# Kernel optimization log

Hardware: AMD Instinct MI355X
Metric: run time of the kernel (lower is better)

Reference implementation:

```python
import jax, jax.numpy as jnp
import numpy as np

N = 100000
E = 1600000
IN_CH = 128
HID = 64      # hidden_channels, heads=1 -> out_ch per head = 64
OUT = 40      # final classes, heads=1, concat=False -> mean over 1 head
SLOPE = 0.2   # leaky relu slope


def setup_inputs() -> dict:
    key = jax.random.key(0)
    k = jax.random.split(key, 6)
    x = jax.random.normal(k[0], (N, IN_CH), dtype=jnp.float32)
    edge_index = jax.random.randint(k[1], (2, E), 0, N, dtype=jnp.int32)
    # xavier-ish scales
    W0 = jax.random.normal(k[2], (HID, IN_CH), dtype=jnp.float32) * (2.0 / (HID + IN_CH)) ** 0.5
    att0 = jax.random.normal(k[3], (1, 1, 2 * HID), dtype=jnp.float32) * 0.1
    W1 = jax.random.normal(k[4], (OUT, HID), dtype=jnp.float32) * (2.0 / (OUT + HID)) ** 0.5
    att1 = jax.random.normal(k[5], (1, 1, 2 * OUT), dtype=jnp.float32) * 0.1
    return {"x": x, "edge_index": edge_index, "W0": W0, "att0": att0, "W1": W1, "att1": att1}


def _gat_conv(h_in, src, dst, W, att, out_ch, concat):
    # h_in: (N, in_ch) -> h: (N, 1, out_ch)   (heads = 1)
    h = (h_in @ W.T).reshape(N, 1, out_ch)
    x_i = h[dst]                                   # (Etot, 1, out_ch) target feats
    x_j = h[src]                                   # (Etot, 1, out_ch) source feats
    logits = jnp.sum(jnp.concatenate([x_i, x_j], axis=-1) * att, axis=-1)  # (Etot, 1)
    logits = jax.nn.leaky_relu(logits, negative_slope=SLOPE)
    # segment softmax over destination node
    m = jax.ops.segment_max(logits, dst, num_segments=N)
    e = jnp.exp(logits - m[dst])
    s = jax.ops.segment_sum(e, dst, num_segments=N)
    alpha = e / s[dst]                             # (Etot, 1)
    out = jax.ops.segment_sum(x_j * alpha[..., None], dst, num_segments=N)  # (N, 1, out_ch)
    return out.reshape(N, out_ch) if concat else out.mean(axis=1)


def reference(x, edge_index, W0, att0, W1, att1):
    # add_self_loops (applied inside each GATConv with the same node count)
    loops = jnp.arange(N, dtype=edge_index.dtype)
    ei = jnp.concatenate([edge_index, jnp.stack([loops, loops])], axis=1)
    src, dst = ei[0], ei[1]  # PyG source_to_target: x_j = x[src], x_i = x[dst]
    h = _gat_conv(x, src, dst, W0, att0, HID, concat=True)
    h = jax.nn.relu(h)  # dropout inactive in eval mode
    h = _gat_conv(h, src, dst, W1, att1, OUT, concat=False)
    return jax.nn.log_softmax(h, axis=1)
```

## Files before the change

kernel.cpp:

```cpp
#include <hip/hip_runtime.h>
#include <math.h>

#define NNODES 100000
#define NEDGES 1600000
#define ETOT   (NEDGES + NNODES)

#define BSZ   128
#define KBUCK ((NNODES + BSZ - 1) / BSZ)
#define CAP   2816
#define NSUB  8
#define CAPS  768
#define CPAD  16

#define GEMMB 1563
#define EPT   4
#define BUCKB ((ETOT + 1024 - 1) / 1024)
#define GGRP  ((GEMMB + 7) / 8)
#define BGRP  ((BUCKB + 7) / 8)

__device__ __forceinline__ int xcc_id() {
    int x;
    asm volatile("s_getreg_b32 %0, hwreg(HW_REG_XCC_ID)" : "=s"(x));
    return x & (NSUB - 1);
}

__device__ __forceinline__ unsigned short f2bf(float f) {
    unsigned u = __float_as_uint(f);
    return (unsigned short)((u + 0x7FFFu + ((u >> 16) & 1u)) >> 16);
}

__global__ void zero_cnt(int* __restrict__ cnt) {
    int i = blockIdx.x * blockDim.x + threadIdx.x;
    if (i < KBUCK * NSUB * CPAD) cnt[i] = 0;
}

__device__ __forceinline__ void bucket_body(int bb, const int* __restrict__ ei,
                                            int* __restrict__ cnt,
                                            unsigned int* __restrict__ stage) {
    const int t = threadIdx.x;
    const int xg = xcc_id();
#pragma unroll
    for (int r = 0; r < EPT; ++r) {
        int e = bb * 1024 + r * 256 + t;
        if (e < ETOT) {
            int src, dst;
            if (e < NEDGES) { src = ei[e]; dst = ei[NEDGES + e]; }
            else            { src = dst = e - NEDGES; }
            int sb = (dst >> 7) * NSUB + xg;
            int pos = atomicAdd(&cnt[sb * CPAD], 1);
            if (pos < CAPS)
                stage[(size_t)sb * CAPS + pos] =
                    ((unsigned)(dst & 127) << 24) | (unsigned)src;
        }
    }
}

__device__ __forceinline__ void gemm0_body(int gb, const float* __restrict__ x,
                                           const float* __restrict__ W,
                                           const float* __restrict__ att,
                                           unsigned short* __restrict__ h0b,
                                           float* __restrict__ ai,
                                           float* __restrict__ aj) {
    __shared__ float Wt[128 * 68];
    const int tid = threadIdx.x;
    const int nb = gb * 64;

    const int lane = tid & 63;
    const int w    = tid >> 6;
    const int ocg  = lane & 15;
    const int ng   = lane >> 4;
    const int nodeLocal = w * 16 + ng * 4;

    const float* xp[4];
#pragma unroll
    for (int j = 0; j < 4; ++j) {
        int node = nb + nodeLocal + j;
        xp[j] = x + (size_t)(node < NNODES ? node : NNODES - 1) * 128;
    }

    float4 xa[4], xb[4], xc[4];
#pragma unroll
    for (int j = 0; j < 4; ++j) {
        xa[j] = *(const float4*)(xp[j] + 0);
        xb[j] = *(const float4*)(xp[j] + 4);
        xc[j] = *(const float4*)(xp[j] + 8);
    }

    for (int i = tid; i < 128 * 64; i += 256) {
        int oc = i >> 7, k = i & 127;
        Wt[k * 68 + oc] = W[i];
    }
    __syncthreads();

    float4 acc[4];
#pragma unroll
    for (int j = 0; j < 4; ++j) acc[j] = make_float4(0.f, 0.f, 0.f, 0.f);

#pragma unroll 4
    for (int k4 = 0; k4 < 32; ++k4) {
        const int kb = k4 * 4;
        int kpf = kb + 12; if (kpf > 124) kpf = 124;
        float4 xn0 = *(const float4*)(xp[0] + kpf);
        float4 xn1 = *(const float4*)(xp[1] + kpf);
        float4 xn2 = *(const float4*)(xp[2] + kpf);
        float4 xn3 = *(const float4*)(xp[3] + kpf);
        float4 wv0 = *(const float4*)&Wt[(kb + 0) * 68 + ocg * 4];
        float4 wv1 = *(const float4*)&Wt[(kb + 1) * 68 + ocg * 4];
        float4 wv2 = *(const float4*)&Wt[(kb + 2) * 68 + ocg * 4];
        float4 wv3 = *(const float4*)&Wt[(kb + 3) * 68 + ocg * 4];
#pragma unroll
        for (int j = 0; j < 4; ++j) {
            float4 xv = xa[j];
            acc[j].x += xv.x * wv0.x + xv.y * wv1.x + xv.z * wv2.x + xv.w * wv3.x;
            acc[j].y += xv.x * wv0.y + xv.y * wv1.y + xv.z * wv2.y + xv.w * wv3.y;
            acc[j].z += xv.x * wv0.z + xv.y * wv1.z + xv.z * wv2.z + xv.w * wv3.z;
            acc[j].w += xv.x * wv0.w + xv.y * wv1.w + xv.z * wv2.w + xv.w * wv3.w;
        }
        xa[0] = xb[0]; xa[1] = xb[1]; xa[2] = xb[2]; xa[3] = xb[3];
        xb[0] = xc[0]; xb[1] = xc[1]; xb[2] = xc[2]; xb[3] = xc[3];
        xc[0] = xn0;   xc[1] = xn1;   xc[2] = xn2;   xc[3] = xn3;
    }

    const int ocb = ocg * 4;
    float ati[4], atj[4];
#pragma unroll
    for (int i = 0; i < 4; ++i) {
        ati[i] = att[ocb + i];
        atj[i] = att[64 + ocb + i];
    }

#pragma unroll
    for (int j = 0; j < 4; ++j) {
        int nodeG = nb + nodeLocal + j;
        float pai = acc[j].x * ati[0] + acc[j].y * ati[1] + acc[j].z * ati[2] + acc[j].w * ati[3];
        float paj = acc[j].x * atj[0] + acc[j].y * atj[1] + acc[j].z * atj[2] + acc[j].w * atj[3];
#pragma unroll
        for (int off = 1; off < 16; off <<= 1) {
            pai += __shfl_xor(pai, off, 64);
            paj += __shfl_xor(paj, off, 64);
        }
        if (nodeG < NNODES) {
            unsigned p0 = ((unsigned)f2bf(acc[j].y) << 16) | f2bf(acc[j].x);
            unsigned p1 = ((unsigned)f2bf(acc[j].w) << 16) | f2bf(acc[j].z);
            *(uint2*)&h0b[(size_t)nodeG * 64 + ocb] = make_uint2(p0, p1);
            if (ocg == 0) { ai[nodeG] = pai; aj[nodeG] = paj; }
        }
    }
}

__global__ __launch_bounds__(256) void fusedA(
        const int* __restrict__ ei, int* __restrict__ cnt,
        unsigned int* __restrict__ stage,
        const float* __restrict__ x, const float* __restrict__ W0,
        const float* __restrict__ att0,
        unsigned short* __restrict__ h0b, float* __restrict__ ai0,
        float* __restrict__ aj0) {
    const int bid = blockIdx.x;
    const int grp = bid >> 3, sub = bid & 7;
    if ((grp & 1) && (grp >> 1) < GGRP) {
        int g = (grp >> 1) * 8 + sub;
        if (g < GEMMB) gemm0_body(g, x, W0, att0, h0b, ai0, aj0);
    } else {
        int bg = grp - min(GGRP, (grp + 1) >> 1);
        int bb = bg * 8 + sub;
        if (bb < BUCKB) bucket_body(bb, ei, cnt, stage);
    }
}

__global__ void bucket_scan(const int* __restrict__ cnt, int* __restrict__ bstart) {
    __shared__ int wsum[16];
    const int t = threadIdx.x;
    int x = 0;
    if (t < KBUCK) {
#pragma unroll
        for (int s = 0; s < NSUB; ++s) x += min(cnt[(t * NSUB + s) * CPAD], CAPS);
    }
    int lane = t & 63, w = t >> 6;
    int inc = x;
#pragma unroll
    for (int off = 1; off < 64; off <<= 1) {
        int u = __shfl_up(inc, off, 64);
        if (lane >= off) inc += u;
    }
    if (lane == 63) wsum[w] = inc;
    __syncthreads();
    if (t == 0) {
        int s = 0;
#pragma unroll
        for (int j = 0; j < 16; ++j) { int y = wsum[j]; wsum[j] = s; s += y; }
    }
    __syncthreads();
    int excl = inc - x + wsum[w];
    if (t < KBUCK) bstart[t] = excl;
    if (t == KBUCK) bstart[KBUCK] = excl;
}

__global__ __launch_bounds__(256) void bucket_scatter(
        const int* __restrict__ cnt, const int* __restrict__ bstart,
        const unsigned int* __restrict__ stage, int* __restrict__ rowstart,
        int* __restrict__ csr_src) {
    __shared__ unsigned int ent[CAP];
    __shared__ int hist[BSZ];
    __shared__ int scnt[NSUB];
    __shared__ int soff[NSUB + 1];
    __shared__ int wtot;
    const int b = blockIdx.x, t = threadIdx.x;
    const int n0 = b * BSZ;
    const int base = bstart[b];

    if (t < BSZ) hist[t] = 0;
    if (t < NSUB) scnt[t] = min(cnt[(b * NSUB + t) * CPAD], CAPS);
    __syncthreads();
    if (t == 0) {
        int s = 0;
#pragma unroll
        for (int x = 0; x < NSUB; ++x) { soff[x] = s; s += scnt[x]; }
        soff[NSUB] = s;
    }
    __syncthreads();

#pragma unroll
    for (int x = 0; x < NSUB; ++x) {
        const int cx = scnt[x];
        const int ox = soff[x];
        const unsigned int* sp = stage + (size_t)(b * NSUB + x) * CAPS;
        for (int i = t; i < cx; i += 256) {
            unsigned int v = sp[i];
            ent[ox + i] = v;
            atomicAdd(&hist[v >> 24], 1);
        }
    }
    __syncthreads();
    const int c = soff[NSUB];

    int lane = t & 63, w = t >> 6;
    int v = (t < BSZ) ? hist[t] : 0;
    int inc = v;
#pragma unroll
    for (int off = 1; off < 64; off <<= 1) {
        int u = __shfl_up(inc, off, 64);
        if (lane >= off) inc += u;
    }
    if (t == 63) wtot = inc;
    __syncthreads();
    int excl = inc - v + ((w == 1) ? wtot : 0);
    if (t < BSZ) {
        int node = n0 + t;
        if (node <= NNODES) rowstart[node] = base + excl;
    }
    __syncthreads();
    if (t < BSZ) hist[t] = excl;
    __syncthreads();
    for (int i = t; i < c; i += 256) {
        unsigned int e = ent[i];
        int pos = atomicAdd(&hist[e >> 24], 1);
        csr_src[base + pos] = (int)(e & 0xFFFFFFu);
    }
}

__global__ __launch_bounds__(256) void agg_gemm1(
        const int* __restrict__ rowstart, const int* __restrict__ csr_src,
        const float* __restrict__ aj,
        const float* __restrict__ ai, const unsigned short* __restrict__ h0b,
        const float* __restrict__ W1, const float* __restrict__ att1,
        unsigned short* __restrict__ h1b, float* __restrict__ ai1,
        float* __restrict__ aj1) {
    __shared__ float  W1L[64 * 68];
    __shared__ float  rowbuf[4][64];

    const int tid = threadIdx.x;
    for (int i = tid; i < 64 * 64; i += 256) {
        int oc = i >> 6, k = i & 63;
        W1L[oc * 68 + k] = (oc < 40) ? W1[oc * 64 + k] : 0.0f;
    }
    __syncthreads();

    const int lane = tid & 63;
    const int wid  = tid >> 6;
    const int n = blockIdx.x * 4 + wid;
    if (n >= NNODES) return;

    const int start = rowstart[n];
    const int end   = rowstart[n + 1];
    const float ain = ai[n];

    const int cg = lane & 7;
    const int sg = lane >> 3;
    const int cgo = cg << 3;
    float4 accA = make_float4(0.f, 0.f, 0.f, 0.f);
    float4 accB = make_float4(0.f, 0.f, 0.f, 0.f);
    float  esum = 0.0f;

    for (int c = start; c < end; c += 64) {
        int rem = end - c;
        int cnt = (rem < 64) ? rem : 64;
        int s = (lane < cnt) ? csr_src[c + lane] : 0;
        for (int j0 = 0; j0 < cnt; j0 += 8) {
            int j  = j0 + sg;
            int sj = __shfl(s, j, 64);
            if (j < cnt) {
                float ajv = aj[sj];
                uint4 hv = *(const uint4*)&h0b[(unsigned)(sj << 6) + cgo];
                float t = ain + ajv;
                t = (t > 0.0f) ? t : 0.2f * t;
                float a = __expf(t);
                esum += a;
                float c0 = __uint_as_float(hv.x << 16);
                float c1 = __uint_as_float(hv.x & 0xFFFF0000u);
                float c2 = __uint_as_float(hv.y << 16);
                float c3 = __uint_as_float(hv.y & 0xFFFF0000u);
                float c4 = __uint_as_float(hv.z << 16);
                float c5 = __uint_as_float(hv.z & 0xFFFF0000u);
                float c6 = __uint_as_float(hv.w << 16);
                float c7 = __uint_as_float(hv.w & 0xFFFF0000u);
                accA.x = fmaf(a, c0, accA.x);
                accA.y = fmaf(a, c1, accA.y);
                accA.z = fmaf(a, c2, accA.z);
                accA.w = fmaf(a, c3, accA.w);
                accB.x = fmaf(a, c4, accB.x);
                accB.y = fmaf(a, c5, accB.y);
                accB.z = fmaf(a, c6, accB.z);
                accB.w = fmaf(a, c7, accB.w);
            }
        }
    }
#pragma unroll
    for (int off = 32; off > 0; off >>= 1) esum += __shfl_xor(esum, off, 64);
    const float inv = 8.0f / esum;
#pragma unroll
    for (int off = 8; off < 64; off <<= 1) {
        accA.x += __shfl_xor(accA.x, off, 64);
        accA.y += __shfl_xor(accA.y, off, 64);
        accA.z += __shfl_xor(accA.z, off, 64);
        accA.w += __shfl_xor(accA.w, off, 64);
        accB.x += __shfl_xor(accB.x, off, 64);
        accB.y += __shfl_xor(accB.y, off, 64);
        accB.z += __shfl_xor(accB.z, off, 64);
        accB.w += __shfl_xor(accB.w, off, 64);
    }
    if (sg == 0) {
        float4 rA, rB;
        rA.x = fmaxf(accA.x * inv, 0.0f);
        rA.y = fmaxf(accA.y * inv, 0.0f);
        rA.z = fmaxf(accA.z * inv, 0.0f);
        rA.w = fmaxf(accA.w * inv, 0.0f);
        rB.x = fmaxf(accB.x * inv, 0.0f);
        rB.y = fmaxf(accB.y * inv, 0.0f);
        rB.z = fmaxf(accB.z * inv, 0.0f);
        rB.w = fmaxf(accB.w * inv, 0.0f);
        *(float4*)&rowbuf[wid][cgo]     = rA;
        *(float4*)&rowbuf[wid][cgo + 4] = rB;
    }

    const int oc = lane;
    float hacc = 0.0f;
#pragma unroll
    for (int k4 = 0; k4 < 16; ++k4) {
        float4 rv = *(const float4*)&rowbuf[wid][k4 * 4];
        float4 wv = *(const float4*)&W1L[oc * 68 + k4 * 4];
        hacc = fmaf(rv.x, wv.x, hacc);
        hacc = fmaf(rv.y, wv.y, hacc);
        hacc = fmaf(rv.z, wv.z, hacc);
        hacc = fmaf(rv.w, wv.w, hacc);
    }

    const bool ocOK = (oc < 40);
    if (ocOK) h1b[(size_t)n * 40 + oc] = f2bf(hacc);
    float pai = ocOK ? hacc * att1[oc]      : 0.0f;
    float paj = ocOK ? hacc * att1[40 + oc] : 0.0f;
#pragma unroll
    for (int off = 1; off < 64; off <<= 1) {
        pai += __shfl_xor(pai, off, 64);
        paj += __shfl_xor(paj, off, 64);
    }
    if (lane == 0) { ai1[n] = pai; aj1[n] = paj; }
}

__global__ __launch_bounds__(256) void agg_lsm(
        const int* __restrict__ rowstart, const int* __restrict__ csr_src,
        const float* __restrict__ aj,
        const float* __restrict__ ai, const unsigned short* __restrict__ h1b,
        float* __restrict__ out) {
    const int lane = threadIdx.x & 63;
    const int wid  = threadIdx.x >> 6;
    const int n = blockIdx.x * 4 + wid;
    if (n >= NNODES) return;

    const int start = rowstart[n];
    const int end   = rowstart[n + 1];
    const float ain = ai[n];

    const int  cg   = lane & 7;
    const int  sg   = lane >> 3;
    const bool chOK = (cg < 5);
    float4 accA = make_float4(0.f, 0.f, 0.f, 0.f);
    float4 accB = make_float4(0.f, 0.f, 0.f, 0.f);
    float  esum = 0.0f;

    for (int c = start; c < end; c += 64) {
        int rem = end - c;
        int cnt = (rem < 64) ? rem : 64;
        int s = (lane < cnt) ? csr_src[c + lane] : 0;
        for (int j0 = 0; j0 < cnt; j0 += 8) {
            int j  = j0 + sg;
            int sj = __shfl(s, j, 64);
            if (j < cnt) {
                float ajv = aj[sj];
                float t = ain + ajv;
                t = (t > 0.0f) ? t : 0.2f * t;
                float a = __expf(t);
                esum += a;
                if (chOK) {
                    uint4 hv = *(const uint4*)&h1b[(unsigned)(sj * 40) + (cg << 3)];
                    float c0 = __uint_as_float(hv.x << 16);
                    float c1 = __uint_as_float(hv.x & 0xFFFF0000u);
                    float c2 = __uint_as_float(hv.y << 16);
                    float c3 = __uint_as_float(hv.y & 0xFFFF0000u);
                    float c4 = __uint_as_float(hv.z << 16);
                    float c5 = __uint_as_float(hv.z & 0xFFFF0000u);
                    float c6 = __uint_as_float(hv.w << 16);
                    float c7 = __uint_as_float(hv.w & 0xFFFF0000u);
                    accA.x = fmaf(a, c0, accA.x);
                    accA.y = fmaf(a, c1, accA.y);
                    accA.z = fmaf(a, c2, accA.z);
                    accA.w = fmaf(a, c3, accA.w);
                    accB.x = fmaf(a, c4, accB.x);
                    accB.y = fmaf(a, c5, accB.y);
                    accB.z = fmaf(a, c6, accB.z);
                    accB.w = fmaf(a, c7, accB.w);
                }
            }
        }
    }
#pragma unroll
    for (int off = 32; off > 0; off >>= 1) esum += __shfl_xor(esum, off, 64);
    const float inv = 8.0f / esum;
#pragma unroll
    for (int off = 8; off < 64; off <<= 1) {
        accA.x += __shfl_xor(accA.x, off, 64);
        accA.y += __shfl_xor(accA.y, off, 64);
        accA.z += __shfl_xor(accA.z, off, 64);
        accA.w += __shfl_xor(accA.w, off, 64);
        accB.x += __shfl_xor(accB.x, off, 64);
        accB.y += __shfl_xor(accB.y, off, 64);
        accB.z += __shfl_xor(accB.z, off, 64);
        accB.w += __shfl_xor(accB.w, off, 64);
    }
    accA.x *= inv; accA.y *= inv; accA.z *= inv; accA.w *= inv;
    accB.x *= inv; accB.y *= inv; accB.z *= inv; accB.w *= inv;

    float mx = -INFINITY;
    if (chOK) {
        mx = fmaxf(fmaxf(fmaxf(accA.x, accA.y), fmaxf(accA.z, accA.w)),
                   fmaxf(fmaxf(accB.x, accB.y), fmaxf(accB.z, accB.w)));
    }
#pragma unroll
    for (int off = 1; off < 8; off <<= 1) mx = fmaxf(mx, __shfl_xor(mx, off, 64));
    float sm = 0.0f;
    if (chOK) {
        sm = __expf(accA.x - mx) + __expf(accA.y - mx) +
             __expf(accA.z - mx) + __expf(accA.w - mx) +
             __expf(accB.x - mx) + __expf(accB.y - mx) +
             __expf(accB.z - mx) + __expf(accB.w - mx);
    }
#pragma unroll
    for (int off = 1; off < 8; off <<= 1) sm += __shfl_xor(sm, off, 64);
    float ls = mx + logf(sm);
    if (sg == 0 && chOK) {
        float4 oA = make_float4(accA.x - ls, accA.y - ls, accA.z - ls, accA.w - ls);
        float4 oB = make_float4(accB.x - ls, accB.y - ls, accB.z - ls, accB.w - ls);
        *(float4*)&out[(size_t)n * 40 + (cg << 3)]     = oA;
        *(float4*)&out[(size_t)n * 40 + (cg << 3) + 4] = oB;
    }
}

extern "C" void kernel_launch(void* const* d_in, const int* in_sizes, int n_in,
                              void* d_out, int out_size, void* d_ws, size_t ws_size,
                              hipStream_t stream) {
    const float* x    = (const float*)d_in[0];
    const int*   ei   = (const int*)  d_in[1];
    const float* W0   = (const float*)d_in[2];
    const float* att0 = (const float*)d_in[3];
    const float* W1   = (const float*)d_in[4];
    const float* att1 = (const float*)d_in[5];
    float* out = (float*)d_out;

    int* wi = (int*)d_ws;
    int*  cnt      = wi;
    int*  bstart   = cnt + 100352;
    int*  rowstart = bstart + 1024;
    unsigned int* stage = (unsigned int*)(rowstart + 100352);
    int*  csr_src  = (int*)(stage + (size_t)KBUCK * NSUB * CAPS);
    unsigned short* h0b = (unsigned short*)(csr_src + 1700096);
    unsigned short* h1b = h0b + (size_t)NNODES * 64;
    float* fbase = (float*)(h1b + (size_t)NNODES * 40);
    float* ai0 = fbase;
    float* aj0 = ai0 + 100352;
    float* ai1 = aj0 + 100352;
    float* aj1 = ai1 + 100352;

    const int B = 256;
    const int aggGrid = (NNODES + 3) / 4;
    const int fusedGrid = (GGRP + BGRP) * 8;

    zero_cnt<<<(KBUCK * NSUB * CPAD + B - 1) / B, B, 0, stream>>>(cnt);
    fusedA<<<fusedGrid, B, 0, stream>>>(ei, cnt, stage, x, W0, att0, h0b, ai0, aj0);
    bucket_scan<<<1, 1024, 0, stream>>>(cnt, bstart);
    bucket_scatter<<<KBUCK, B, 0, stream>>>(cnt, bstart, stage, rowstart, csr_src);

    agg_gemm1<<<aggGrid, B, 0, stream>>>(rowstart, csr_src, aj0, ai0, h0b,
                                         W1, att1, h1b, ai1, aj1);

    agg_lsm<<<aggGrid, B, 0, stream>>>(rowstart, csr_src, aj1, ai1, h1b, out);
}
```

Before: 378.5 us.

## Precompute per-edge attention exponentials into CSR arrays before aggregation

Computes the unnormalized attention weight exp(leakyrelu(ai+aj)) per edge once: layer 0 inside bucket_scatter, layer 1 in a new alpha1_k kernel. The results are stored alongside csr_src. The aggregation kernels then read a coalesced alpha value and broadcast it by shuffle. This removes the redundant per-lane exp evaluation, which previously ran once per channel group (hence the old 8/esum factor), and the scattered aj gather inside the aggregation loop. The cost is an extra kernel launch and extra CSR-sized float traffic, and the stage buffer is reused as storage for the layer-1 alphas.

```diff
diff --git a/kernel.cpp b/kernel.cpp
--- a/kernel.cpp
+++ b/kernel.cpp
@@ -198,9 +198,11 @@
 __global__ __launch_bounds__(256) void bucket_scatter(
         const int* __restrict__ cnt, const int* __restrict__ bstart,
         const unsigned int* __restrict__ stage, int* __restrict__ rowstart,
-        int* __restrict__ csr_src) {
+        int* __restrict__ csr_src, float* __restrict__ csr_alpha,
+        const float* __restrict__ ai, const float* __restrict__ aj) {
     __shared__ unsigned int ent[CAP];
     __shared__ int hist[BSZ];
+    __shared__ float aiL[BSZ];
     __shared__ int scnt[NSUB];
     __shared__ int soff[NSUB + 1];
     __shared__ int wtot;
@@ -208,7 +210,11 @@
     const int n0 = b * BSZ;
     const int base = bstart[b];
 
-    if (t < BSZ) hist[t] = 0;
+    if (t < BSZ) {
+        hist[t] = 0;
+        int node = n0 + t;
+        aiL[t] = (node < NNODES) ? ai[node] : 0.0f;
+    }
     if (t < NSUB) scnt[t] = min(cnt[(b * NSUB + t) * CPAD], CAPS);
     __syncthreads();
     if (t == 0) {
@@ -253,15 +259,38 @@
     __syncthreads();
     for (int i = t; i < c; i += 256) {
         unsigned int e = ent[i];
-        int pos = atomicAdd(&hist[e >> 24], 1);
-        csr_src[base + pos] = (int)(e & 0xFFFFFFu);
+        int dl  = e >> 24;
+        int src = (int)(e & 0xFFFFFFu);
+        int pos = atomicAdd(&hist[dl], 1);
+        float tv = aiL[dl] + aj[src];
+        tv = (tv > 0.0f) ? tv : 0.2f * tv;
+        csr_src[base + pos]   = src;
+        csr_alpha[base + pos] = __expf(tv);
+    }
+}
+
+__global__ __launch_bounds__(256) void alpha1_k(
+        const int* __restrict__ rowstart, const int* __restrict__ csr_src,
+        const float* __restrict__ ai1, const float* __restrict__ aj1,
+        float* __restrict__ csr_alpha2) {
+    const int lane = threadIdx.x & 63;
+    const int wid  = threadIdx.x >> 6;
+    const int n = blockIdx.x * 4 + wid;
+    if (n >= NNODES) return;
+    const int start = rowstart[n];
+    const int end   = rowstart[n + 1];
+    const float ain = ai1[n];
+    for (int c = start + lane; c < end; c += 64) {
+        int s = csr_src[c];
+        float t = ain + aj1[s];
+        t = (t > 0.0f) ? t : 0.2f * t;
+        csr_alpha2[c] = __expf(t);
     }
 }
 
 __global__ __launch_bounds__(256) void agg_gemm1(
         const int* __restrict__ rowstart, const int* __restrict__ csr_src,
-        const float* __restrict__ aj,
-        const float* __restrict__ ai, const unsigned short* __restrict__ h0b,
+        const float* __restrict__ csr_alpha, const unsigned short* __restrict__ h0b,
         const float* __restrict__ W1, const float* __restrict__ att1,
         unsigned short* __restrict__ h1b, float* __restrict__ ai1,
         float* __restrict__ aj1) {
@@ -282,7 +311,6 @@
 
     const int start = rowstart[n];
     const int end   = rowstart[n + 1];
-    const float ain = ai[n];
 
     const int cg = lane & 7;
     const int sg = lane >> 3;
@@ -294,17 +322,19 @@
     for (int c = start; c < end; c += 64) {
         int rem = end - c;
         int cnt = (rem < 64) ? rem : 64;
-        int s = (lane < cnt) ? csr_src[c + lane] : 0;
+        int   s  = 0;
+        float av = 0.0f;
+        if (lane < cnt) {
+            s  = csr_src[c + lane];
+            av = csr_alpha[c + lane];
+        }
+        esum += av;
         for (int j0 = 0; j0 < cnt; j0 += 8) {
             int j  = j0 + sg;
-            int sj = __shfl(s, j, 64);
+            int   sj = __shfl(s,  j, 64);
+            float a  = __shfl(av, j, 64);
             if (j < cnt) {
-                float ajv = aj[sj];
                 uint4 hv = *(const uint4*)&h0b[(unsigned)(sj << 6) + cgo];
-                float t = ain + ajv;
-                t = (t > 0.0f) ? t : 0.2f * t;
-                float a = __expf(t);
-                esum += a;
                 float c0 = __uint_as_float(hv.x << 16);
                 float c1 = __uint_as_float(hv.x & 0xFFFF0000u);
                 float c2 = __uint_as_float(hv.y << 16);
@@ -326,7 +356,7 @@
     }
 #pragma unroll
     for (int off = 32; off > 0; off >>= 1) esum += __shfl_xor(esum, off, 64);
-    const float inv = 8.0f / esum;
+    const float inv = 1.0f / esum;
 #pragma unroll
     for (int off = 8; off < 64; off <<= 1) {
         accA.x += __shfl_xor(accA.x, off, 64);
@@ -378,9 +408,8 @@
 
 __global__ __launch_bounds__(256) void agg_lsm(
         const int* __restrict__ rowstart, const int* __restrict__ csr_src,
-        const float* __restrict__ aj,
-        const float* __restrict__ ai, const unsigned short* __restrict__ h1b,
-        float* __restrict__ out) {
+        const float* __restrict__ csr_alpha2,
+        const unsigned short* __restrict__ h1b, float* __restrict__ out) {
     const int lane = threadIdx.x & 63;
     const int wid  = threadIdx.x >> 6;
     const int n = blockIdx.x * 4 + wid;
@@ -388,7 +417,6 @@
 
     const int start = rowstart[n];
     const int end   = rowstart[n + 1];
-    const float ain = ai[n];
 
     const int  cg   = lane & 7;
     const int  sg   = lane >> 3;
@@ -400,41 +428,41 @@
     for (int c = start; c < end; c += 64) {
         int rem = end - c;
         int cnt = (rem < 64) ? rem : 64;
-        int s = (lane < cnt) ? csr_src[c + lane] : 0;
+        int   s  = 0;
+        float av = 0.0f;
+        if (lane < cnt) {
+            s  = csr_src[c + lane];
+            av = csr_alpha2[c + lane];
+        }
+        esum += av;
         for (int j0 = 0; j0 < cnt; j0 += 8) {
             int j  = j0 + sg;
-            int sj = __shfl(s, j, 64);
-            if (j < cnt) {
-                float ajv = aj[sj];
-                float t = ain + ajv;
-                t = (t > 0.0f) ? t : 0.2f * t;
-                float a = __expf(t);
-                esum += a;
-                if (chOK) {
-                    uint4 hv = *(const uint4*)&h1b[(unsigned)(sj * 40) + (cg << 3)];
-                    float c0 = __uint_as_float(hv.x << 16);
-                    float c1 = __uint_as_float(hv.x & 0xFFFF0000u);
-                    float c2 = __uint_as_float(hv.y << 16);
-                    float c3 = __uint_as_float(hv.y & 0xFFFF0000u);
-                    float c4 = __uint_as_float(hv.z << 16);
-                    float c5 = __uint_as_float(hv.z & 0xFFFF0000u);
-                    float c6 = __uint_as_float(hv.w << 16);
-                    float c7 = __uint_as_float(hv.w & 0xFFFF0000u);
-                    accA.x = fmaf(a, c0, accA.x);
-                    accA.y = fmaf(a, c1, accA.y);
-                    accA.z = fmaf(a, c2, accA.z);
-                    accA.w = fmaf(a, c3, accA.w);
-                    accB.x = fmaf(a, c4, accB.x);
-                    accB.y = fmaf(a, c5, accB.y);
-                    accB.z = fmaf(a, c6, accB.z);
-                    accB.w = fmaf(a, c7, accB.w);
-                }
+            int   sj = __shfl(s,  j, 64);
+            float a  = __shfl(av, j, 64);
+            if (chOK && j < cnt) {
+                uint4 hv = *(const uint4*)&h1b[(unsigned)(sj * 40) + (cg << 3)];
+                float c0 = __uint_as_float(hv.x << 16);
+                float c1 = __uint_as_float(hv.x & 0xFFFF0000u);
+                float c2 = __uint_as_float(hv.y << 16);
+                float c3 = __uint_as_float(hv.y & 0xFFFF0000u);
+                float c4 = __uint_as_float(hv.z << 16);
+                float c5 = __uint_as_float(hv.z & 0xFFFF0000u);
+                float c6 = __uint_as_float(hv.w << 16);
+                float c7 = __uint_as_float(hv.w & 0xFFFF0000u);
+                accA.x = fmaf(a, c0, accA.x);
+                accA.y = fmaf(a, c1, accA.y);
+                accA.z = fmaf(a, c2, accA.z);
+                accA.w = fmaf(a, c3, accA.w);
+                accB.x = fmaf(a, c4, accB.x);
+                accB.y = fmaf(a, c5, accB.y);
+                accB.z = fmaf(a, c6, accB.z);
+                accB.w = fmaf(a, c7, accB.w);
             }
         }
     }
 #pragma unroll
     for (int off = 32; off > 0; off >>= 1) esum += __shfl_xor(esum, off, 64);
-    const float inv = 8.0f / esum;
+    const float inv = 1.0f / esum;
 #pragma unroll
     for (int off = 8; off < 64; off <<= 1) {
         accA.x += __shfl_xor(accA.x, off, 64);
@@ -491,13 +519,15 @@
     int*  rowstart = bstart + 1024;
     unsigned int* stage = (unsigned int*)(rowstart + 100352);
     int*  csr_src  = (int*)(stage + (size_t)KBUCK * NSUB * CAPS);
-    unsigned short* h0b = (unsigned short*)(csr_src + 1700096);
+    float* csr_alpha = (float*)(csr_src + 1700096);
+    unsigned short* h0b = (unsigned short*)(csr_alpha + 1700096);
     unsigned short* h1b = h0b + (size_t)NNODES * 64;
     float* fbase = (float*)(h1b + (size_t)NNODES * 40);
     float* ai0 = fbase;
     float* aj0 = ai0 + 100352;
     float* ai1 = aj0 + 100352;
     float* aj1 = ai1 + 100352;
+    float* csr_alpha2 = (float*)stage;
 
     const int B = 256;
     const int aggGrid = (NNODES + 3) / 4;
@@ -506,10 +536,12 @@
     zero_cnt<<<(KBUCK * NSUB * CPAD + B - 1) / B, B, 0, stream>>>(cnt);
     fusedA<<<fusedGrid, B, 0, stream>>>(ei, cnt, stage, x, W0, att0, h0b, ai0, aj0);
     bucket_scan<<<1, 1024, 0, stream>>>(cnt, bstart);
-    bucket_scatter<<<KBUCK, B, 0, stream>>>(cnt, bstart, stage, rowstart, csr_src);
-
-    agg_gemm1<<<aggGrid, B, 0, stream>>>(rowstart, csr_src, aj0, ai0, h0b,
+    bucket_scatter<<<KBUCK, B, 0, stream>>>(cnt, bstart, stage, rowstart,
+                                            csr_src, csr_alpha, ai0, aj0);
+
+    agg_gemm1<<<aggGrid, B, 0, stream>>>(rowstart, csr_src, csr_alpha, h0b,
                                          W1, att1, h1b, ai1, aj1);
 
-    agg_lsm<<<aggGrid, B, 0, stream>>>(rowstart, csr_src, aj1, ai1, h1b, out);
-}
+    alpha1_k<<<aggGrid, B, 0, stream>>>(rowstart, csr_src, ai1, aj1, csr_alpha2);
+    agg_lsm<<<aggGrid, B, 0, stream>>>(rowstart, csr_src, csr_alpha2, h1b, out);
+}
```

New measurement: 402.3 us. 1.06x slower.
